# Kernel tuning notes

Hardware: AMD Instinct MI355X
Metric: run time of the kernel (lower is better)

## Reference

```python
import jax, jax.numpy as jnp
import numpy as np

# SMPL-style skeleton: parent index per joint (parent < child, root = -1)
PARENTS = [-1, 0, 0, 0, 1, 2, 3, 4, 5, 6, 7, 8, 9, 9, 9, 12, 13, 14, 16, 17, 18, 19, 20, 21]
END_SITES = [10, 11, 15, 22, 23]  # feet, head, hands
NUM_JOINTS = len(PARENTS)


def rot6d_to_matrix(x):
    """6D rotation rep -> 3x3 matrix via Gram-Schmidt. x: [..., 6] -> [..., 3, 3].
    eye(3).reshape(-1)[:6] = [1,0,0,0,1,0] maps to identity under this (row-stacked) convention."""
    a1, a2 = x[..., 0:3], x[..., 3:6]
    b1 = a1 / jnp.linalg.norm(a1, axis=-1, keepdims=True)
    a2p = a2 - jnp.sum(b1 * a2, axis=-1, keepdims=True) * b1
    b2 = a2p / jnp.linalg.norm(a2p, axis=-1, keepdims=True)
    b3 = jnp.cross(b1, b2)
    return jnp.stack([b1, b2, b3], axis=-2)


def fk_positions(rot, offsets):
    """Forward kinematics (faithful to _recompute_joint_global_info).
    rot: [F, J, 3, 3] local joint rotations; offsets: [F, J, 3].
    Returns global joint positions [F, J, 3]. Loop is over the fixed, small
    joint hierarchy (structural), fully vectorized over frames."""
    positions = [offsets[:, 0]]          # root: offset only
    orientations = [rot[:, 0]]           # root: local rotation
    for i in range(1, NUM_JOINTS):
        pi = PARENTS[i]
        po = orientations[pi]            # [F, 3, 3]
        pos = jnp.einsum('fab,fb->fa', po, offsets[:, i]) + positions[pi]
        positions.append(pos)
        orientations.append(po @ rot[:, i])
    return jnp.stack(positions, axis=1)  # [F, J, 3]


def setup_inputs() -> dict:
    key = jax.random.key(0)
    ks = jax.random.split(key, 6)
    F = 65536
    return {
        'poseA': jax.random.normal(ks[0], (F, NUM_JOINTS, 6), dtype=jnp.float32),
        'poseB': jax.random.normal(ks[1], (F, NUM_JOINTS, 6), dtype=jnp.float32),
        'joint_offsets_A': jax.random.normal(ks[2], (F, NUM_JOINTS, 3), dtype=jnp.float32),
        'joint_offsets_B': jax.random.normal(ks[3], (F, NUM_JOINTS, 3), dtype=jnp.float32),
        't_poseA': jax.random.normal(ks[4], (NUM_JOINTS, 3), dtype=jnp.float32),
        't_poseB': jax.random.normal(ks[5], (NUM_JOINTS, 3), dtype=jnp.float32),
    }


def reference(poseA, poseB, joint_offsets_A, joint_offsets_B, t_poseA, t_poseB):
    ee = jnp.array(END_SITES)
    # 6D -> rotation matrices (to_matrix)
    RA = rot6d_to_matrix(poseA)
    RB = rot6d_to_matrix(poseB)
    # sequential per-joint FK (the hot loop)
    posA = fk_positions(RA, joint_offsets_A)
    posB = fk_positions(RB, joint_offsets_B)
    # bbox scale from T-pose
    scale_A = jnp.max(t_poseA, axis=0) - jnp.min(t_poseA, axis=0)  # [3]
    scale_B = jnp.max(t_poseB, axis=0) - jnp.min(t_poseB, axis=0)
    eeA = posA[:, ee, :] - t_poseA[ee, :]   # [F, E, 3]
    eeB = posB[:, ee, :] - t_poseB[ee, :]
    loss = jnp.mean((eeA / scale_A - eeB / scale_B) ** 2)
    return loss
```

## Files before the change

### kernel.cpp

```cpp
#include <hip/hip_runtime.h>


struct V3 { float x, y, z; };
struct M3 { float m[3][3]; };

__device__ __forceinline__ V3 matvec(const M3& A, const V3& v) {
    return { A.m[0][0]*v.x + A.m[0][1]*v.y + A.m[0][2]*v.z,
             A.m[1][0]*v.x + A.m[1][1]*v.y + A.m[1][2]*v.z,
             A.m[2][0]*v.x + A.m[2][1]*v.y + A.m[2][2]*v.z };
}

__device__ __forceinline__ M3 matmul(const M3& A, const M3& B) {
    M3 C;
#pragma unroll
    for (int i = 0; i < 3; i++)
#pragma unroll
        for (int j = 0; j < 3; j++)
            C.m[i][j] = A.m[i][0]*B.m[0][j] + A.m[i][1]*B.m[1][j] + A.m[i][2]*B.m[2][j];
    return C;
}

#define PROW 25
#define OROW 13

struct FK { M3 o; V3 p; };

__device__ __forceinline__ M3 rot6d_lds(const float* __restrict__ rp, int base) {
    float v0 = rp[base+0], v1 = rp[base+1], v2 = rp[base+2];
    float v3 = rp[base+3], v4 = rp[base+4], v5 = rp[base+5];
    float n1 = v0*v0 + v1*v1 + v2*v2;
    float r1 = 1.0f / sqrtf(n1);
    V3 b1 = { v0*r1, v1*r1, v2*r1 };
    float d = b1.x*v3 + b1.y*v4 + b1.z*v5;
    V3 u = { v3 - d*b1.x, v4 - d*b1.y, v5 - d*b1.z };
    float n2 = u.x*u.x + u.y*u.y + u.z*u.z;
    float r2 = 1.0f / sqrtf(n2);
    V3 b2 = { u.x*r2, u.y*r2, u.z*r2 };
    V3 b3 = { b1.y*b2.z - b1.z*b2.y, b1.z*b2.x - b1.x*b2.z, b1.x*b2.y - b1.y*b2.x };
    M3 R;
    R.m[0][0]=b1.x; R.m[0][1]=b1.y; R.m[0][2]=b1.z;
    R.m[1][0]=b2.x; R.m[1][1]=b2.y; R.m[1][2]=b2.z;
    R.m[2][0]=b3.x; R.m[2][1]=b3.y; R.m[2][2]=b3.z;
    return R;
}

__device__ __forceinline__ FK fk_step_l(const float* __restrict__ rp,
                                        const float* __restrict__ ro,
                                        int pb, int ob, const FK& par) {
    V3 off = { ro[ob], ro[ob+1], ro[ob+2] };
    V3 t = matvec(par.o, off);
    FK s;
    s.p = { par.p.x + t.x, par.p.y + t.y, par.p.z + t.z };
    s.o = matmul(par.o, rot6d_lds(rp, pb));
    return s;
}

__device__ __forceinline__ V3 fk_end_l(const float* __restrict__ ro,
                                       int ob, const FK& par) {
    V3 off = { ro[ob], ro[ob+1], ro[ob+2] };
    V3 t = matvec(par.o, off);
    return { par.p.x + t.x, par.p.y + t.y, par.p.z + t.z };
}

__global__ __launch_bounds__(256)
void ee_loss_kernel(const float* __restrict__ poseA, const float* __restrict__ poseB,
                    const float* __restrict__ offA,  const float* __restrict__ offB,
                    const float* __restrict__ tA,    const float* __restrict__ tB,
                    float* __restrict__ out, float inv_count) {
    __shared__ float s_pose[4][64 * PROW];
    __shared__ float s_off [4][64 * OROW];
    __shared__ float s_eeB[128][15];
    __shared__ float s_inv[6];
    __shared__ float s_d[15];
    __shared__ float s_part[2];

    const int tid  = threadIdx.x;
    const int wid  = tid >> 6;
    const int lane = tid & 63;
    const bool isB = wid & 1;
    const int fg   = wid >> 1;
    const int fl   = fg * 64 + lane;
    const long long f0 = (long long)blockIdx.x * 128 + fg * 64;

    const float* __restrict__ P = (isB ? poseB : poseA) + f0 * 144;
    const float* __restrict__ O = (isB ? offB  : offA ) + f0 * 72;

    float* sp = s_pose[wid];
    float* so = s_off[wid];
    const float* rp = sp + lane * PROW;
    const float* ro = so + lane * OROW;

    if (tid < 6) {
        const float* tp = (tid < 3) ? tA : tB;
        int ax = (tid < 3) ? tid : tid - 3;
        float mn = tp[ax], mx = mn;
#pragma unroll
        for (int j = 1; j < 24; j++) {
            float v = tp[j*3 + ax];
            mn = fminf(mn, v); mx = fmaxf(mx, v);
        }
        s_inv[tid] = 1.0f / (mx - mn);
    }
    if (tid < 15) {
        const int EE[5] = {10, 11, 15, 22, 23};
        int e = tid / 3, ax = tid - 3*e;
        int j = EE[e];
        float mnA = tA[ax], mxA = mnA, mnB = tB[ax], mxB = mnB;
#pragma unroll
        for (int k = 1; k < 24; k++) {
            float a = tA[k*3 + ax], b = tB[k*3 + ax];
            mnA = fminf(mnA, a); mxA = fmaxf(mxA, a);
            mnB = fminf(mnB, b); mxB = fmaxf(mxB, b);
        }
        s_d[tid] = tB[j*3 + ax]/(mxB - mnB) - tA[j*3 + ax]/(mxA - mnA);
    }

    auto stageP = [&](int st) {
#pragma unroll
        for (int k = 0; k < 6; k++) {
            int idx = lane + 64 * k;
            int f = idx / 6, c = idx - 6 * f;
            float4 v = *(const float4*)(P + f*144 + st*24 + c*4);
            float* d = sp + f*PROW + c*4;
            d[0] = v.x; d[1] = v.y; d[2] = v.z; d[3] = v.w;
        }
#pragma unroll
        for (int k = 0; k < 6; k++) {
            int idx = lane + 64 * k;
            int f = idx / 6, c = idx - 6 * f;
            float2 v = *(const float2*)(O + f*72 + st*12 + c*2);
            float* d = so + f*OROW + c*2;
            d[0] = v.x; d[1] = v.y;
        }
    };

    stageP(0);
    FK s0; s0.o = rot6d_lds(rp, 0); s0.p = { ro[0], ro[1], ro[2] };
    FK s1 = fk_step_l(rp, ro,  6, 3, s0);
    FK s2 = fk_step_l(rp, ro, 12, 6, s0);
    FK s3 = fk_step_l(rp, ro, 18, 9, s0);

    stageP(1);
    FK s4 = fk_step_l(rp, ro,  0, 0, s1);
    FK s5 = fk_step_l(rp, ro,  6, 3, s2);
    FK s6 = fk_step_l(rp, ro, 12, 6, s3);
    FK s7 = fk_step_l(rp, ro, 18, 9, s4);

    stageP(2);
    FK s8 = fk_step_l(rp, ro,  0, 0, s5);
    FK s9 = fk_step_l(rp, ro,  6, 3, s6);
    V3 e10 = fk_end_l(ro, 6, s7);
    V3 e11 = fk_end_l(ro, 9, s8);

    stageP(3);
    FK s12 = fk_step_l(rp, ro,  0, 0, s9);
    FK s13 = fk_step_l(rp, ro,  6, 3, s9);
    FK s14 = fk_step_l(rp, ro, 12, 6, s9);
    V3 e15 = fk_end_l(ro, 9, s12);

    stageP(4);
    FK s16 = fk_step_l(rp, ro,  0, 0, s13);
    FK s17 = fk_step_l(rp, ro,  6, 3, s14);
    FK s18 = fk_step_l(rp, ro, 12, 6, s16);
    FK s19 = fk_step_l(rp, ro, 18, 9, s17);

    stageP(5);
    FK s20 = fk_step_l(rp, ro,  0, 0, s18);
    FK s21 = fk_step_l(rp, ro,  6, 3, s19);
    V3 e22 = fk_end_l(ro, 6, s20);
    V3 e23 = fk_end_l(ro, 9, s21);

    if (isB) {
        s_eeB[fl][ 0] = e10.x; s_eeB[fl][ 1] = e10.y; s_eeB[fl][ 2] = e10.z;
        s_eeB[fl][ 3] = e11.x; s_eeB[fl][ 4] = e11.y; s_eeB[fl][ 5] = e11.z;
        s_eeB[fl][ 6] = e15.x; s_eeB[fl][ 7] = e15.y; s_eeB[fl][ 8] = e15.z;
        s_eeB[fl][ 9] = e22.x; s_eeB[fl][10] = e22.y; s_eeB[fl][11] = e22.z;
        s_eeB[fl][12] = e23.x; s_eeB[fl][13] = e23.y; s_eeB[fl][14] = e23.z;
    }
    __syncthreads();

    float local = 0.0f;
    if (!isB) {
        const float iax = s_inv[0], iay = s_inv[1], iaz = s_inv[2];
        const float ibx = s_inv[3], iby = s_inv[4], ibz = s_inv[5];
        const float* eb = s_eeB[fl];
        float t0  = e10.x*iax - eb[ 0]*ibx + s_d[ 0];
        float t1  = e10.y*iay - eb[ 1]*iby + s_d[ 1];
        float t2  = e10.z*iaz - eb[ 2]*ibz + s_d[ 2];
        float t3  = e11.x*iax - eb[ 3]*ibx + s_d[ 3];
        float t4  = e11.y*iay - eb[ 4]*iby + s_d[ 4];
        float t5  = e11.z*iaz - eb[ 5]*ibz + s_d[ 5];
        float t6  = e15.x*iax - eb[ 6]*ibx + s_d[ 6];
        float t7  = e15.y*iay - eb[ 7]*iby + s_d[ 7];
        float t8  = e15.z*iaz - eb[ 8]*ibz + s_d[ 8];
        float t9  = e22.x*iax - eb[ 9]*ibx + s_d[ 9];
        float t10 = e22.y*iay - eb[10]*iby + s_d[10];
        float t11 = e22.z*iaz - eb[11]*ibz + s_d[11];
        float t12 = e23.x*iax - eb[12]*ibx + s_d[12];
        float t13 = e23.y*iay - eb[13]*iby + s_d[13];
        float t14 = e23.z*iaz - eb[14]*ibz + s_d[14];
        local = ((t0*t0 + t1*t1) + (t2*t2 + t3*t3) + (t4*t4 + t5*t5) +
                 (t6*t6 + t7*t7) + (t8*t8 + t9*t9) + (t10*t10 + t11*t11) +
                 (t12*t12 + t13*t13) + t14*t14) * inv_count;
#pragma unroll
        for (int off = 32; off > 0; off >>= 1)
            local += __shfl_down(local, off, 64);
        if (lane == 0) s_part[fg] = local;
    }
    __syncthreads();
    if (tid == 0) atomicAdd(out, s_part[0] + s_part[1]);
}

extern "C" void kernel_launch(void* const* d_in, const int* in_sizes, int n_in,
                              void* d_out, int out_size, void* d_ws, size_t ws_size,
                              hipStream_t stream) {
    const float* poseA = (const float*)d_in[0];
    const float* poseB = (const float*)d_in[1];
    const float* offA  = (const float*)d_in[2];
    const float* offB  = (const float*)d_in[3];
    const float* tA    = (const float*)d_in[4];
    const float* tB    = (const float*)d_in[5];
    float* out = (float*)d_out;

    const int F = in_sizes[0] / 144;
    const int blocks = F / 128;
    const float inv_count = 1.0f / ((float)F * 15.0f);

    hipMemsetAsync(out, 0, sizeof(float), stream);
    ee_loss_kernel<<<blocks, 256, 0, stream>>>(poseA, poseB, offA, offB, tA, tB,
                                               out, inv_count);
}
```

Before: 147.3 us.

## Stage eight joints per step with register-prefetched double-buffered global loads

Joint data is staged into LDS in three chunks of eight joints instead of six chunks of four. Global loads for the next chunk are issued into registers ahead of time, with sched_barrier fences, so memory latency overlaps the forward-kinematics math. The end-effector exchange buffer now reuses the pose LDS region behind a barrier. LDS per block and VGPR use both grow, which can lower occupancy.

Result: no change. 147.6 us (+0.2%).

```diff
diff --git a/kernel.cpp b/kernel.cpp
--- a/kernel.cpp
+++ b/kernel.cpp
@@ -20,8 +20,8 @@
     return C;
 }
 
-#define PROW 25
-#define OROW 13
+#define PROW 49
+#define OROW 25
 
 struct FK { M3 o; V3 p; };
 
@@ -69,7 +69,6 @@
                     float* __restrict__ out, float inv_count) {
     __shared__ float s_pose[4][64 * PROW];
     __shared__ float s_off [4][64 * OROW];
-    __shared__ float s_eeB[128][15];
     __shared__ float s_inv[6];
     __shared__ float s_d[15];
     __shared__ float s_part[2];
@@ -115,61 +114,80 @@
         s_d[tid] = tB[j*3 + ax]/(mxB - mnB) - tA[j*3 + ax]/(mxA - mnA);
     }
 
-    auto stageP = [&](int st) {
+    auto gload = [&](float4* cp, float4* co, int st) {
+#pragma unroll
+        for (int k = 0; k < 12; k++) {
+            int idx = lane + 64 * k;
+            int f = idx / 12, c = idx - 12 * f;
+            cp[k] = *(const float4*)(P + f*144 + st*48 + c*4);
+        }
 #pragma unroll
         for (int k = 0; k < 6; k++) {
             int idx = lane + 64 * k;
             int f = idx / 6, c = idx - 6 * f;
-            float4 v = *(const float4*)(P + f*144 + st*24 + c*4);
+            co[k] = *(const float4*)(O + f*72 + st*24 + c*4);
+        }
+    };
+    auto swrite = [&](const float4* cp, const float4* co) {
+#pragma unroll
+        for (int k = 0; k < 12; k++) {
+            int idx = lane + 64 * k;
+            int f = idx / 12, c = idx - 12 * f;
             float* d = sp + f*PROW + c*4;
-            d[0] = v.x; d[1] = v.y; d[2] = v.z; d[3] = v.w;
+            d[0] = cp[k].x; d[1] = cp[k].y; d[2] = cp[k].z; d[3] = cp[k].w;
         }
 #pragma unroll
         for (int k = 0; k < 6; k++) {
             int idx = lane + 64 * k;
             int f = idx / 6, c = idx - 6 * f;
-            float2 v = *(const float2*)(O + f*72 + st*12 + c*2);
-            float* d = so + f*OROW + c*2;
-            d[0] = v.x; d[1] = v.y;
+            float* d = so + f*OROW + c*4;
+            d[0] = co[k].x; d[1] = co[k].y; d[2] = co[k].z; d[3] = co[k].w;
         }
     };
 
-    stageP(0);
+    float4 cpA[12], coA[6];
+    float4 cpB[12], coB[6];
+
+    gload(cpA, coA, 0);
+    gload(cpB, coB, 1);
+    __builtin_amdgcn_sched_barrier(0);
+    swrite(cpA, coA);
+
     FK s0; s0.o = rot6d_lds(rp, 0); s0.p = { ro[0], ro[1], ro[2] };
-    FK s1 = fk_step_l(rp, ro,  6, 3, s0);
-    FK s2 = fk_step_l(rp, ro, 12, 6, s0);
-    FK s3 = fk_step_l(rp, ro, 18, 9, s0);
-
-    stageP(1);
-    FK s4 = fk_step_l(rp, ro,  0, 0, s1);
-    FK s5 = fk_step_l(rp, ro,  6, 3, s2);
-    FK s6 = fk_step_l(rp, ro, 12, 6, s3);
-    FK s7 = fk_step_l(rp, ro, 18, 9, s4);
-
-    stageP(2);
-    FK s8 = fk_step_l(rp, ro,  0, 0, s5);
-    FK s9 = fk_step_l(rp, ro,  6, 3, s6);
-    V3 e10 = fk_end_l(ro, 6, s7);
-    V3 e11 = fk_end_l(ro, 9, s8);
-
-    stageP(3);
-    FK s12 = fk_step_l(rp, ro,  0, 0, s9);
-    FK s13 = fk_step_l(rp, ro,  6, 3, s9);
-    FK s14 = fk_step_l(rp, ro, 12, 6, s9);
-    V3 e15 = fk_end_l(ro, 9, s12);
-
-    stageP(4);
-    FK s16 = fk_step_l(rp, ro,  0, 0, s13);
-    FK s17 = fk_step_l(rp, ro,  6, 3, s14);
-    FK s18 = fk_step_l(rp, ro, 12, 6, s16);
-    FK s19 = fk_step_l(rp, ro, 18, 9, s17);
-
-    stageP(5);
-    FK s20 = fk_step_l(rp, ro,  0, 0, s18);
-    FK s21 = fk_step_l(rp, ro,  6, 3, s19);
-    V3 e22 = fk_end_l(ro, 6, s20);
-    V3 e23 = fk_end_l(ro, 9, s21);
-
+    FK s1 = fk_step_l(rp, ro,  6,  3, s0);
+    FK s2 = fk_step_l(rp, ro, 12,  6, s0);
+    FK s3 = fk_step_l(rp, ro, 18,  9, s0);
+    FK s4 = fk_step_l(rp, ro, 24, 12, s1);
+    FK s5 = fk_step_l(rp, ro, 30, 15, s2);
+    FK s6 = fk_step_l(rp, ro, 36, 18, s3);
+    FK s7 = fk_step_l(rp, ro, 42, 21, s4);
+
+    swrite(cpB, coB);
+    gload(cpA, coA, 2);
+    __builtin_amdgcn_sched_barrier(0);
+
+    FK s8  = fk_step_l(rp, ro,  0,  0, s5);
+    FK s9  = fk_step_l(rp, ro,  6,  3, s6);
+    V3 e10 = fk_end_l(ro,  6, s7);
+    V3 e11 = fk_end_l(ro,  9, s8);
+    FK s12 = fk_step_l(rp, ro, 24, 12, s9);
+    FK s13 = fk_step_l(rp, ro, 30, 15, s9);
+    FK s14 = fk_step_l(rp, ro, 36, 18, s9);
+    V3 e15 = fk_end_l(ro, 21, s12);
+
+    swrite(cpA, coA);
+
+    FK s16 = fk_step_l(rp, ro,  0,  0, s13);
+    FK s17 = fk_step_l(rp, ro,  6,  3, s14);
+    FK s18 = fk_step_l(rp, ro, 12,  6, s16);
+    FK s19 = fk_step_l(rp, ro, 18,  9, s17);
+    FK s20 = fk_step_l(rp, ro, 24, 12, s18);
+    FK s21 = fk_step_l(rp, ro, 30, 15, s19);
+    V3 e22 = fk_end_l(ro, 18, s20);
+    V3 e23 = fk_end_l(ro, 21, s21);
+
+    float (*s_eeB)[15] = (float (*)[15])(&s_pose[0][0]);
+    __syncthreads();
     if (isB) {
         s_eeB[fl][ 0] = e10.x; s_eeB[fl][ 1] = e10.y; s_eeB[fl][ 2] = e10.z;
         s_eeB[fl][ 3] = e11.x; s_eeB[fl][ 4] = e11.y; s_eeB[fl][ 5] = e11.z;
```
